# Kernel optimization log

Hardware: AMD Instinct MI355X
Metric: run time of the kernel (lower is better)

Reference implementation:

```python
import jax, jax.numpy as jnp
import numpy as np
import math

HEADS = 4
DIM_HEAD = 32
EPS = 1e-5

def _ln_channels(x):
    # LayerNorm over channel axis (axis=1) of NCHW, no affine (eps=1e-5)
    mu = jnp.mean(x, axis=1, keepdims=True)
    var = jnp.mean((x - mu) ** 2, axis=1, keepdims=True)
    return (x - mu) * jax.lax.rsqrt(var + EPS)

def setup_inputs() -> dict:
    key = jax.random.key(0)
    k1, k2, k3, k4 = jax.random.split(key, 4)
    dim, inner = 256, HEADS * DIM_HEAD
    x = jax.random.normal(k1, (16, dim, 64, 64), dtype=jnp.float32)
    Wqkv = jax.random.normal(k2, (3 * inner, dim), dtype=jnp.float32) * (1.0 / math.sqrt(dim))
    Wout = jax.random.normal(k3, (dim, inner), dtype=jnp.float32) * (1.0 / math.sqrt(inner))
    bout = jax.random.normal(k4, (dim,), dtype=jnp.float32) * 0.01
    return {"x": x, "Wqkv": Wqkv, "Wout": Wout, "bout": bout}

def reference(x, Wqkv, Wout, bout):
    B, C, H, W = x.shape
    N = H * W
    inner = HEADS * DIM_HEAD
    # pre-norm (channel-wise LayerNorm via permute in torch)
    normed = _ln_channels(x)
    # 1x1 conv to qkv: [B, 3*inner, H, W]
    qkv = jnp.einsum('oc,bchw->bohw', Wqkv, normed)
    q, k, v = jnp.split(qkv, 3, axis=1)
    # [B, inner, H, W] -> [B, heads, N, dim_head]
    def to_heads(t):
        return t.reshape(B, HEADS, DIM_HEAD, N).transpose(0, 1, 3, 2)
    q, k, v = to_heads(q), to_heads(k), to_heads(v)
    q = jax.nn.softmax(q, axis=-1)          # over dim_head
    k = jax.nn.softmax(k, axis=-2)          # over N
    q = q / math.sqrt(DIM_HEAD)
    v = v / N
    context = jnp.einsum('bhnd,bhne->bhde', k, v)   # [B,h,d,d]
    out = jnp.einsum('bhde,bhnd->bhne', context, q) # [B,h,N,d]
    out = out.transpose(0, 1, 3, 2).reshape(B, inner, H, W)
    out = jnp.einsum('oc,bchw->bohw', Wout, out) + bout[None, :, None, None]
    out = _ln_channels(out)                  # LinearAttention.out_norm
    return out + x                           # residual
```

## Files before the change

### kernel.cpp

```cpp
#include <hip/hip_runtime.h>
#include <hip/hip_bf16.h>
#include <math.h>

#define BATCH 16
#define CH 256
#define NPOS 4096
#define INNER 128
#define HEADS 4
#define DH 32

typedef __hip_bfloat16 bf16;
typedef short bf8v __attribute__((ext_vector_type(8)));
typedef float f32x4 __attribute__((ext_vector_type(4)));

__device__ __forceinline__ float b2f(bf16 v) { return __bfloat162float(v); }
__device__ __forceinline__ float us2f(unsigned short u) {
    unsigned w = ((unsigned)u) << 16; float f; __builtin_memcpy(&f, &w, 4); return f;
}
__device__ __forceinline__ unsigned short f2us(float f) {
    bf16 h = __float2bfloat16(f); unsigned short u; __builtin_memcpy(&u, &h, 2); return u;
}
__device__ __forceinline__ bf16 f2b(float v) { return __float2bfloat16(v); }

__global__ __launch_bounds__(256)
void prep_w_kernel(const float* __restrict__ Wqkv, bf16* __restrict__ wqb) {
    int idx = (blockIdx.x * 256 + threadIdx.x) * 4;
    float4 w = *(const float4*)&Wqkv[idx];
    ushort4 u;
    u.x = f2us(w.x); u.y = f2us(w.y); u.z = f2us(w.z); u.w = f2us(w.w);
    *(ushort4*)&wqb[idx] = u;
}

__global__ __launch_bounds__(256)
void fused_qkv_kernel(const float* __restrict__ x, const bf16* __restrict__ wqb,
                      bf16* __restrict__ p, bf16* __restrict__ kvt) {
    __shared__ bf16 A[64 * 264];
    __shared__ float stats[512];

    const int b = blockIdx.y, n0 = blockIdx.x * 64;
    const int tid = threadIdx.x;
    const int w = tid >> 6, lane = tid & 63;
    const int lrow = lane & 15, kq = lane >> 4;

    {
        const int n = tid & 63, cq = tid >> 6;
        const float* xp = x + ((size_t)b * CH + cq * 64) * NPOS + n0 + n;
        float s = 0.f, sq = 0.f;
        for (int i0 = 0; i0 < 64; i0 += 8) {
            bf8v bv;
            #pragma unroll
            for (int j = 0; j < 8; ++j) {
                float v = xp[(size_t)(i0 + j) * NPOS];
                s += v; sq += v * v;
                bv[j] = (short)f2us(v);
            }
            *(bf8v*)&A[n * 264 + cq * 64 + i0] = bv;
        }
        stats[tid * 2] = s; stats[tid * 2 + 1] = sq;
    }
    __syncthreads();
    if (tid < 64) {
        float s  = stats[tid * 2]     + stats[(tid + 64) * 2]
                 + stats[(tid + 128) * 2] + stats[(tid + 192) * 2];
        float sq = stats[tid * 2 + 1] + stats[(tid + 64) * 2 + 1]
                 + stats[(tid + 128) * 2 + 1] + stats[(tid + 192) * 2 + 1];
        float m = s * (1.f / 256.f);
        float var = sq * (1.f / 256.f) - m * m;
        stats[tid * 2] = m;
        stats[tid * 2 + 1] = rsqrtf(var + 1e-5f);
    }
    __syncthreads();
    {
        unsigned* A32 = (unsigned*)A;
        #pragma unroll 4
        for (int i = 0; i < 32; ++i) {
            int idx = i * 256 + tid;
            int c2 = idx & 127, n = idx >> 7;
            unsigned u = A32[n * 132 + c2];
            float m = stats[n * 2], rs = stats[n * 2 + 1];
            float v0 = (us2f((unsigned short)(u & 0xffffu)) - m) * rs;
            float v1 = (us2f((unsigned short)(u >> 16)) - m) * rs;
            A32[n * 132 + c2] = (unsigned)f2us(v0) | ((unsigned)f2us(v1) << 16);
        }
    }
    __syncthreads();

    for (int ph = 0; ph < 3; ++ph) {
        const int colbase = (ph == 2) ? 0 : (ph + 1) * 128;
        const bf16* wp = wqb + (size_t)(colbase + w * 32) * 256;
        f32x4 acc[4][2];
        #pragma unroll
        for (int i = 0; i < 4; ++i) {
            acc[i][0] = (f32x4){0.f, 0.f, 0.f, 0.f};
            acc[i][1] = (f32x4){0.f, 0.f, 0.f, 0.f};
        }

        #pragma unroll 2
        for (int k0 = 0; k0 < 256; k0 += 32) {
            bf8v af[4], bfr[2];
            #pragma unroll
            for (int t = 0; t < 4; ++t)
                af[t] = *(const bf8v*)&A[(t * 16 + lrow) * 264 + k0 + kq * 8];
            #pragma unroll
            for (int t = 0; t < 2; ++t)
                bfr[t] = *(const bf8v*)&wp[(size_t)(t * 16 + lrow) * 256 + k0 + kq * 8];
            #pragma unroll
            for (int mt = 0; mt < 4; ++mt)
                #pragma unroll
                for (int nt = 0; nt < 2; ++nt)
                    acc[mt][nt] = __builtin_amdgcn_mfma_f32_16x16x32_bf16(
                        af[mt], bfr[nt], acc[mt][nt], 0, 0, 0);
        }

        if (ph < 2) {
            #pragma unroll
            for (int mt = 0; mt < 4; ++mt)
                #pragma unroll
                for (int nt = 0; nt < 2; ++nt)
                    #pragma unroll
                    for (int r = 0; r < 4; ++r) {
                        int row = mt * 16 + kq * 4 + r;
                        int col = w * 32 + nt * 16 + lrow;
                        kvt[(size_t)(b * NPOS + n0 + row) * 256 + ph * 128 + col] =
                            f2b(acc[mt][nt][r]);
                    }
        } else {
            #pragma unroll
            for (int mt = 0; mt < 4; ++mt)
                #pragma unroll
                for (int r = 0; r < 4; ++r) {
                    float e0 = __expf(b2f(f2b(acc[mt][0][r])));
                    float e1 = __expf(b2f(f2b(acc[mt][1][r])));
                    float s = e0 + e1;
                    #pragma unroll
                    for (int m = 1; m <= 8; m <<= 1) s += __shfl_xor(s, m, 64);
                    float rd = 1.f / s;
                    int row = mt * 16 + kq * 4 + r;
                    bf16* pr_ = p + (size_t)(b * NPOS + n0 + row) * 128 + w * 32 + lrow;
                    pr_[0]  = f2b(e0 * rd);
                    pr_[16] = f2b(e1 * rd);
                }
        }
    }
}

__global__ __launch_bounds__(256)
void context_kernel(const bf16* __restrict__ kvt, float* __restrict__ ctxu,
                    float* __restrict__ separt) {
    __shared__ float ks[128][36];
    __shared__ float vs[128][36];
    __shared__ float red_se[4][32];
    int sp = blockIdx.x, h = blockIdx.y, b = blockIdx.z;
    int tid = threadIdx.x;
    int wave = tid >> 6, lane = tid & 63;
    int eg = lane & 7, dg = lane >> 3;
    int sd = tid & 31, sq = (tid >> 5) & 3;
    const int koff = h * DH, voff = 128 + h * DH;
    size_t rowbase = ((size_t)b * NPOS + sp * 1024) * 256;

    float acc[4][4] = {};
    float se_loc = 0.f;

    for (int nc = 0; nc < 1024; nc += 128) {
        for (int t = tid; t < 1024; t += 256) {
            int n = t >> 3, dq = t & 7;
            const bf16* row = kvt + rowbase + (size_t)(nc + n) * 256;
            ushort4 ku = *(const ushort4*)(row + koff + dq * 4);
            ushort4 vu = *(const ushort4*)(row + voff + dq * 4);
            f32x4 kf, vf;
            kf[0] = __expf(us2f(ku.x)); kf[1] = __expf(us2f(ku.y));
            kf[2] = __expf(us2f(ku.z)); kf[3] = __expf(us2f(ku.w));
            vf[0] = us2f(vu.x); vf[1] = us2f(vu.y); vf[2] = us2f(vu.z); vf[3] = us2f(vu.w);
            *(f32x4*)&ks[n][dq * 4] = kf;
            *(f32x4*)&vs[n][dq * 4] = vf;
        }
        __syncthreads();
        #pragma unroll 4
        for (int i = 0; i < 32; ++i) {
            int n = wave * 32 + i;
            f32x4 kv = *(const f32x4*)&ks[n][dg * 4];
            f32x4 vv = *(const f32x4*)&vs[n][eg * 4];
            #pragma unroll
            for (int j = 0; j < 4; ++j)
                #pragma unroll
                for (int i2 = 0; i2 < 4; ++i2)
                    acc[j][i2] += kv[j] * vv[i2];
        }
        if (tid < 128) {
            float s = 0.f;
            #pragma unroll 8
            for (int i = 0; i < 32; ++i) s += ks[sq * 32 + i][sd];
            se_loc += s;
        }
        __syncthreads();
    }

    if (tid < 128) red_se[sq][sd] = se_loc;
    float* red = &ks[0][0];
    #pragma unroll
    for (int j = 0; j < 4; ++j)
        #pragma unroll
        for (int i = 0; i < 4; ++i)
            red[(wave * 64 + lane) * 16 + j * 4 + i] = acc[j][i];
    __syncthreads();
    size_t bhsp = ((size_t)(b * HEADS + h) * 4 + sp);
    for (int idx = tid; idx < 1024; idx += 256) {
        int d = idx >> 5, e = idx & 31;
        int l = (d >> 2) * 8 + (e >> 2);
        int slot = (d & 3) * 4 + (e & 3);
        float s = 0.f;
        #pragma unroll
        for (int w = 0; w < 4; ++w) s += red[(w * 64 + l) * 16 + slot];
        ctxu[bhsp * 1024 + idx] = s;
    }
    if (tid < 32) {
        float s = red_se[0][tid] + red_se[1][tid] + red_se[2][tid] + red_se[3][tid];
        separt[bhsp * 32 + tid] = s;
    }
}

__global__ __launch_bounds__(256)
void wmod_kernel(const float* __restrict__ Wout, const float* __restrict__ ctxu,
                 const float* __restrict__ separt, bf16* __restrict__ wmod) {
    __shared__ float cs[4096];
    __shared__ float ses[128];
    int cg = blockIdx.x, b = blockIdx.y;
    int tid = threadIdx.x;
    for (int idx = tid; idx < 4096; idx += 256) {
        int hh = idx >> 10, rest = idx & 1023;
        float s = 0.f;
        #pragma unroll
        for (int sp = 0; sp < 4; ++sp)
            s += ctxu[(((size_t)(b * HEADS + hh) * 4) + sp) * 1024 + rest];
        cs[idx] = s;
    }
    if (tid < 128) {
        int hh = tid >> 5, d = tid & 31;
        float s = 0.f;
        #pragma unroll
        for (int sp = 0; sp < 4; ++sp)
            s += separt[(((size_t)(b * HEADS + hh) * 4) + sp) * 32 + d];
        ses[tid] = s;
    }
    __syncthreads();
    int c = cg * 32 + (tid & 31);
    int g = tid >> 5;
    int h = g >> 1, d0 = (g & 1) * 16;
    const float* wr = Wout + (size_t)c * INNER + h * DH;
    float w[32];
    #pragma unroll
    for (int i = 0; i < 8; ++i) {
        float4 t = *(const float4*)&wr[i * 4];
        w[i * 4] = t.x; w[i * 4 + 1] = t.y; w[i * 4 + 2] = t.z; w[i * 4 + 3] = t.w;
    }
    const float SCALE = 4.3158341e-05f;
    #pragma unroll
    for (int dd = 0; dd < 16; ++dd) {
        int d = d0 + dd;
        const float* cr = &cs[h * 1024 + d * 32];
        float s = 0.f;
        #pragma unroll
        for (int e4 = 0; e4 < 8; ++e4) {
            f32x4 t = *(const f32x4*)&cr[e4 * 4];
            s += w[e4 * 4] * t[0] + w[e4 * 4 + 1] * t[1]
               + w[e4 * 4 + 2] * t[2] + w[e4 * 4 + 3] * t[3];
        }
        float val = s * SCALE / ses[h * 32 + d];
        wmod[((size_t)b * CH + c) * INNER + h * DH + d] = f2b(val);
    }
}

__global__ __launch_bounds__(256)
void fused_out_kernel(const bf16* __restrict__ p, const bf16* __restrict__ wmod,
                      const float* __restrict__ bout, const float* __restrict__ x,
                      float* __restrict__ out) {
    __shared__ char lds[36864];
    bf16* Ap = (bf16*)lds;
    float* ct = (float*)lds;
    float* st = (float*)(lds + 33792);

    const int b = blockIdx.y, n0 = blockIdx.x * 64;
    const int tid = threadIdx.x;
    const int w = tid >> 6, lane = tid & 63;
    const int lrow = lane & 15, kq = lane >> 4;

    {
        const unsigned* pg32 = (const unsigned*)p;
        unsigned* A32 = (unsigned*)Ap;
        #pragma unroll 4
        for (int i = 0; i < 16; ++i) {
            int idx = i * 256 + tid;
            int c2 = idx & 63, n = idx >> 6;
            A32[n * 68 + c2] = pg32[(size_t)(b * NPOS + n0 + n) * 64 + c2];
        }
    }
    __syncthreads();

    f32x4 acc[4][4];
    #pragma unroll
    for (int i = 0; i < 4; ++i)
        #pragma unroll
        for (int j = 0; j < 4; ++j) acc[i][j] = (f32x4){0.f, 0.f, 0.f, 0.f};

    const bf16* wb = wmod + (size_t)b * CH * INNER + (size_t)(w * 64) * INNER;
    #pragma unroll 2
    for (int k0 = 0; k0 < 128; k0 += 32) {
        bf8v af[4], bfr[4];
        #pragma unroll
        for (int t = 0; t < 4; ++t)
            af[t] = *(const bf8v*)&Ap[(t * 16 + lrow) * 136 + k0 + kq * 8];
        #pragma unroll
        for (int t = 0; t < 4; ++t)
            bfr[t] = *(const bf8v*)&wb[(size_t)(t * 16 + lrow) * 128 + k0 + kq * 8];
        #pragma unroll
        for (int mt = 0; mt < 4; ++mt)
            #pragma unroll
            for (int nt = 0; nt < 4; ++nt)
                acc[mt][nt] = __builtin_amdgcn_mfma_f32_16x16x32_bf16(
                    af[mt], bfr[nt], acc[mt][nt], 0, 0, 0);
    }

    #pragma unroll
    for (int nt = 0; nt < 4; ++nt) {
        float bv = bout[w * 64 + nt * 16 + lrow];
        #pragma unroll
        for (int mt = 0; mt < 4; ++mt)
            #pragma unroll
            for (int r = 0; r < 4; ++r) acc[mt][nt][r] += bv;
    }

    #pragma unroll
    for (int mt = 0; mt < 4; ++mt)
        #pragma unroll
        for (int r = 0; r < 4; ++r) {
            float s = 0.f, sq = 0.f;
            #pragma unroll
            for (int nt = 0; nt < 4; ++nt) {
                float v = acc[mt][nt][r];
                s += v; sq += v * v;
            }
            #pragma unroll
            for (int m = 1; m <= 8; m <<= 1) {
                s += __shfl_xor(s, m, 64);
                sq += __shfl_xor(sq, m, 64);
            }
            if (lrow == 0) {
                int row = mt * 16 + kq * 4 + r;
                st[w * 128 + row * 2] = s;
                st[w * 128 + row * 2 + 1] = sq;
            }
        }
    __syncthreads();
    if (tid < 64) {
        float s  = st[tid * 2]     + st[128 + tid * 2]
                 + st[256 + tid * 2] + st[384 + tid * 2];
        float sq = st[tid * 2 + 1] + st[128 + tid * 2 + 1]
                 + st[256 + tid * 2 + 1] + st[384 + tid * 2 + 1];
        float m = s * (1.f / 256.f);
        float var = sq * (1.f / 256.f) - m * m;
        st[512 + tid * 2] = m;
        st[512 + tid * 2 + 1] = rsqrtf(var + 1e-5f);
    }
    __syncthreads();
    #pragma unroll
    for (int mt = 0; mt < 4; ++mt)
        #pragma unroll
        for (int r = 0; r < 4; ++r) {
            int row = mt * 16 + kq * 4 + r;
            float m = st[512 + row * 2], rs = st[512 + row * 2 + 1];
            #pragma unroll
            for (int nt = 0; nt < 4; ++nt)
                acc[mt][nt][r] = (acc[mt][nt][r] - m) * rs;
        }

    for (int pr = 0; pr < 2; ++pr) {
        __syncthreads();
        #pragma unroll
        for (int mi = 0; mi < 2; ++mi) {
            int mt = pr * 2 + mi;
            #pragma unroll
            for (int nt = 0; nt < 4; ++nt)
                #pragma unroll
                for (int r = 0; r < 4; ++r) {
                    int rl = mi * 16 + kq * 4 + r;
                    ct[(w * 64 + nt * 16 + lrow) * 33 + rl] = acc[mt][nt][r];
                }
        }
        __syncthreads();
        #pragma unroll 4
        for (int i = 0; i < 32; ++i) {
            int idx = i * 256 + tid;
            int n = idx & 31, c = idx >> 5;
            size_t gi = ((size_t)b * CH + c) * NPOS + n0 + pr * 32 + n;
            out[gi] = ct[c * 33 + n] + x[gi];
        }
    }
}

extern "C" void kernel_launch(void* const* d_in, const int* in_sizes, int n_in,
                              void* d_out, int out_size, void* d_ws, size_t ws_size,
                              hipStream_t stream) {
    const float* x    = (const float*)d_in[0];
    const float* Wqkv = (const float*)d_in[1];
    const float* Wout = (const float*)d_in[2];
    const float* bout = (const float*)d_in[3];
    float* out = (float*)d_out;

    char* ws = (char*)d_ws;
    bf16*  p      = (bf16*)ws;
    bf16*  kvt    = (bf16*)(ws + 16777216);
    float* ctxu   = (float*)(ws + 50331648);
    float* separt = (float*)(ws + 51380224);
    bf16*  wmod   = (bf16*)(ws + 51412992);
    bf16*  wqb    = (bf16*)(ws + 50331648);

    prep_w_kernel<<<dim3(96), 256, 0, stream>>>(Wqkv, wqb);
    fused_qkv_kernel<<<dim3(64, BATCH), 256, 0, stream>>>(x, wqb, p, kvt);
    context_kernel<<<dim3(4, HEADS, BATCH), 256, 0, stream>>>(kvt, ctxu, separt);
    wmod_kernel<<<dim3(8, BATCH), 256, 0, stream>>>(Wout, ctxu, separt, wmod);
    fused_out_kernel<<<dim3(64, BATCH), 256, 0, stream>>>(p, wmod, bout, x, out);
}
```

Before: 211.6 us.

## Fuse k/v context computation into QKV kernel via per-tile MFMA partials

```diff
diff --git a/kernel.cpp b/kernel.cpp
--- a/kernel.cpp
+++ b/kernel.cpp
@@ -33,41 +33,51 @@
 
 __global__ __launch_bounds__(256)
 void fused_qkv_kernel(const float* __restrict__ x, const bf16* __restrict__ wqb,
-                      bf16* __restrict__ p, bf16* __restrict__ kvt) {
-    __shared__ bf16 A[64 * 264];
-    __shared__ float stats[512];
-
-    const int b = blockIdx.y, n0 = blockIdx.x * 64;
+                      bf16* __restrict__ p, float* __restrict__ ctxp) {
+    __shared__ char smem[36864];
+    __shared__ float stats[640];
+
+    const int b = blockIdx.y, tile = blockIdx.x, n0 = tile * 64;
     const int tid = threadIdx.x;
     const int w = tid >> 6, lane = tid & 63;
     const int lrow = lane & 15, kq = lane >> 4;
+    bf16* A = (bf16*)smem;
 
     {
-        const int n = tid & 63, cq = tid >> 6;
-        const float* xp = x + ((size_t)b * CH + cq * 64) * NPOS + n0 + n;
-        float s = 0.f, sq = 0.f;
-        for (int i0 = 0; i0 < 64; i0 += 8) {
-            bf8v bv;
-            #pragma unroll
-            for (int j = 0; j < 8; ++j) {
-                float v = xp[(size_t)(i0 + j) * NPOS];
-                s += v; sq += v * v;
-                bv[j] = (short)f2us(v);
-            }
-            *(bf8v*)&A[n * 264 + cq * 64 + i0] = bv;
-        }
-        stats[tid * 2] = s; stats[tid * 2 + 1] = sq;
+        const int nq = tid & 15, cp = tid >> 4;
+        float s[4] = {0.f,0.f,0.f,0.f}, sq[4] = {0.f,0.f,0.f,0.f};
+        #pragma unroll
+        for (int i = 0; i < 8; ++i) {
+            int c0 = cp * 2 + 32 * i;
+            const float* xp = x + ((size_t)b * CH + c0) * NPOS + n0 + nq * 4;
+            float4 fa = *(const float4*)xp;
+            float4 fb = *(const float4*)(xp + NPOS);
+            #pragma unroll
+            for (int j = 0; j < 4; ++j) {
+                float va = (&fa.x)[j], vb = (&fb.x)[j];
+                s[j] += va + vb; sq[j] += va * va + vb * vb;
+                *(unsigned*)&A[(nq * 4 + j) * 264 + c0] =
+                    (unsigned)f2us(va) | ((unsigned)f2us(vb) << 16);
+            }
+        }
+        #pragma unroll
+        for (int j = 0; j < 4; ++j) {
+            s[j]  += __shfl_xor(s[j], 16, 64);  sq[j] += __shfl_xor(sq[j], 16, 64);
+            s[j]  += __shfl_xor(s[j], 32, 64);  sq[j] += __shfl_xor(sq[j], 32, 64);
+            if (lane < 16) {
+                stats[(nq * 4 + j) * 8 + w * 2]     = s[j];
+                stats[(nq * 4 + j) * 8 + w * 2 + 1] = sq[j];
+            }
+        }
     }
     __syncthreads();
     if (tid < 64) {
-        float s  = stats[tid * 2]     + stats[(tid + 64) * 2]
-                 + stats[(tid + 128) * 2] + stats[(tid + 192) * 2];
-        float sq = stats[tid * 2 + 1] + stats[(tid + 64) * 2 + 1]
-                 + stats[(tid + 128) * 2 + 1] + stats[(tid + 192) * 2 + 1];
+        float s  = stats[tid*8] + stats[tid*8+2] + stats[tid*8+4] + stats[tid*8+6];
+        float sq = stats[tid*8+1] + stats[tid*8+3] + stats[tid*8+5] + stats[tid*8+7];
         float m = s * (1.f / 256.f);
         float var = sq * (1.f / 256.f) - m * m;
-        stats[tid * 2] = m;
-        stats[tid * 2 + 1] = rsqrtf(var + 1e-5f);
+        stats[512 + tid * 2] = m;
+        stats[512 + tid * 2 + 1] = rsqrtf(var + 1e-5f);
     }
     __syncthreads();
     {
@@ -77,7 +87,7 @@
             int idx = i * 256 + tid;
             int c2 = idx & 127, n = idx >> 7;
             unsigned u = A32[n * 132 + c2];
-            float m = stats[n * 2], rs = stats[n * 2 + 1];
+            float m = stats[512 + n * 2], rs = stats[512 + n * 2 + 1];
             float v0 = (us2f((unsigned short)(u & 0xffffu)) - m) * rs;
             float v1 = (us2f((unsigned short)(u >> 16)) - m) * rs;
             A32[n * 132 + c2] = (unsigned)f2us(v0) | ((unsigned)f2us(v1) << 16);
@@ -85,16 +95,17 @@
     }
     __syncthreads();
 
+    ushort4 ekp[4][2];
+    float se0 = 0.f, se1 = 0.f;
+
     for (int ph = 0; ph < 3; ++ph) {
-        const int colbase = (ph == 2) ? 0 : (ph + 1) * 128;
-        const bf16* wp = wqb + (size_t)(colbase + w * 32) * 256;
+        const bf16* wp = wqb + (size_t)(ph * 128 + w * 32) * 256;
         f32x4 acc[4][2];
         #pragma unroll
         for (int i = 0; i < 4; ++i) {
-            acc[i][0] = (f32x4){0.f, 0.f, 0.f, 0.f};
-            acc[i][1] = (f32x4){0.f, 0.f, 0.f, 0.f};
-        }
-
+            acc[i][0] = (f32x4){0.f,0.f,0.f,0.f};
+            acc[i][1] = (f32x4){0.f,0.f,0.f,0.f};
+        }
         #pragma unroll 2
         for (int k0 = 0; k0 < 256; k0 += 32) {
             bf8v af[4], bfr[2];
@@ -112,19 +123,8 @@
                         af[mt], bfr[nt], acc[mt][nt], 0, 0, 0);
         }
 
-        if (ph < 2) {
-            #pragma unroll
-            for (int mt = 0; mt < 4; ++mt)
-                #pragma unroll
-                for (int nt = 0; nt < 2; ++nt)
-                    #pragma unroll
-                    for (int r = 0; r < 4; ++r) {
-                        int row = mt * 16 + kq * 4 + r;
-                        int col = w * 32 + nt * 16 + lrow;
-                        kvt[(size_t)(b * NPOS + n0 + row) * 256 + ph * 128 + col] =
-                            f2b(acc[mt][nt][r]);
-                    }
-        } else {
+        if (ph == 0) {
+            unsigned* pg32 = (unsigned*)p;
             #pragma unroll
             for (int mt = 0; mt < 4; ++mt)
                 #pragma unroll
@@ -132,90 +132,96 @@
                     float e0 = __expf(b2f(f2b(acc[mt][0][r])));
                     float e1 = __expf(b2f(f2b(acc[mt][1][r])));
                     float s = e0 + e1;
-                    #pragma unroll
-                    for (int m = 1; m <= 8; m <<= 1) s += __shfl_xor(s, m, 64);
+                    s += __shfl_xor(s, 1, 64);  s += __shfl_xor(s, 2, 64);
+                    s += __shfl_xor(s, 4, 64);  s += __shfl_xor(s, 8, 64);
                     float rd = 1.f / s;
                     int row = mt * 16 + kq * 4 + r;
-                    bf16* pr_ = p + (size_t)(b * NPOS + n0 + row) * 128 + w * 32 + lrow;
-                    pr_[0]  = f2b(e0 * rd);
-                    pr_[16] = f2b(e1 * rd);
+                    pg32[(size_t)(b * NPOS + n0 + row) * 64 + w * 16 + lrow] =
+                        (unsigned)f2us(e0 * rd) | ((unsigned)f2us(e1 * rd) << 16);
                 }
+        } else if (ph == 1) {
+            se0 = 0.f; se1 = 0.f;
+            #pragma unroll
+            for (int mt = 0; mt < 4; ++mt) {
+                ushort4 u0, u1;
+                unsigned short q_;
+                #pragma unroll
+                for (int r = 0; r < 4; ++r) {
+                    q_ = f2us(__expf(b2f(f2b(acc[mt][0][r]))));
+                    se0 += us2f(q_); (&u0.x)[r] = q_;
+                    q_ = f2us(__expf(b2f(f2b(acc[mt][1][r]))));
+                    se1 += us2f(q_); (&u1.x)[r] = q_;
+                }
+                ekp[mt][0] = u0; ekp[mt][1] = u1;
+            }
+            se0 += __shfl_xor(se0, 16, 64); se0 += __shfl_xor(se0, 32, 64);
+            se1 += __shfl_xor(se1, 16, 64); se1 += __shfl_xor(se1, 32, 64);
+        } else {
+            __syncthreads();
+            bf16* ekt = (bf16*)(smem + w * 9216);
+            bf16* vt  = (bf16*)(smem + w * 9216 + 4608);
+            #pragma unroll
+            for (int mt = 0; mt < 4; ++mt)
+                #pragma unroll
+                for (int nt = 0; nt < 2; ++nt) {
+                    ushort4 vv;
+                    vv.x = f2us(acc[mt][nt][0]); vv.y = f2us(acc[mt][nt][1]);
+                    vv.z = f2us(acc[mt][nt][2]); vv.w = f2us(acc[mt][nt][3]);
+                    int d = nt * 16 + lrow, n = mt * 16 + kq * 4;
+                    *(ushort4*)&vt[d * 72 + n]  = vv;
+                    *(ushort4*)&ekt[d * 72 + n] = ekp[mt][nt];
+                }
+            f32x4 cacc[2][2];
+            cacc[0][0] = (f32x4){0.f,0.f,0.f,0.f}; cacc[0][1] = cacc[0][0];
+            cacc[1][0] = cacc[0][0];               cacc[1][1] = cacc[0][0];
+            #pragma unroll
+            for (int ks = 0; ks < 2; ++ks) {
+                bf8v a2[2], bv2[2];
+                a2[0]  = *(const bf8v*)&ekt[lrow * 72 + ks * 32 + kq * 8];
+                a2[1]  = *(const bf8v*)&ekt[(16 + lrow) * 72 + ks * 32 + kq * 8];
+                bv2[0] = *(const bf8v*)&vt[lrow * 72 + ks * 32 + kq * 8];
+                bv2[1] = *(const bf8v*)&vt[(16 + lrow) * 72 + ks * 32 + kq * 8];
+                #pragma unroll
+                for (int mt2 = 0; mt2 < 2; ++mt2)
+                    #pragma unroll
+                    for (int nt2 = 0; nt2 < 2; ++nt2)
+                        cacc[mt2][nt2] = __builtin_amdgcn_mfma_f32_16x16x32_bf16(
+                            a2[mt2], bv2[nt2], cacc[mt2][nt2], 0, 0, 0);
+            }
+            float* pb = ctxp + ((size_t)(b * 64 + tile) * 4 + w) * 1056;
+            #pragma unroll
+            for (int mt2 = 0; mt2 < 2; ++mt2)
+                #pragma unroll
+                for (int nt2 = 0; nt2 < 2; ++nt2)
+                    #pragma unroll
+                    for (int r = 0; r < 4; ++r) {
+                        int d = mt2 * 16 + kq * 4 + r, e = nt2 * 16 + lrow;
+                        pb[d * 32 + e] = cacc[mt2][nt2][r];
+                    }
+            if (kq == 0) {
+                pb[1024 + lrow] = se0;
+                pb[1024 + 16 + lrow] = se1;
+            }
         }
     }
 }
 
 __global__ __launch_bounds__(256)
-void context_kernel(const bf16* __restrict__ kvt, float* __restrict__ ctxu,
-                    float* __restrict__ separt) {
-    __shared__ float ks[128][36];
-    __shared__ float vs[128][36];
-    __shared__ float red_se[4][32];
-    int sp = blockIdx.x, h = blockIdx.y, b = blockIdx.z;
+void reduce_ctx_kernel(const float* __restrict__ ctxp, float* __restrict__ ctxu,
+                       float* __restrict__ separt) {
+    int h = blockIdx.x, b = blockIdx.y;
     int tid = threadIdx.x;
-    int wave = tid >> 6, lane = tid & 63;
-    int eg = lane & 7, dg = lane >> 3;
-    int sd = tid & 31, sq = (tid >> 5) & 3;
-    const int koff = h * DH, voff = 128 + h * DH;
-    size_t rowbase = ((size_t)b * NPOS + sp * 1024) * 256;
-
-    float acc[4][4] = {};
-    float se_loc = 0.f;
-
-    for (int nc = 0; nc < 1024; nc += 128) {
-        for (int t = tid; t < 1024; t += 256) {
-            int n = t >> 3, dq = t & 7;
-            const bf16* row = kvt + rowbase + (size_t)(nc + n) * 256;
-            ushort4 ku = *(const ushort4*)(row + koff + dq * 4);
-            ushort4 vu = *(const ushort4*)(row + voff + dq * 4);
-            f32x4 kf, vf;
-            kf[0] = __expf(us2f(ku.x)); kf[1] = __expf(us2f(ku.y));
-            kf[2] = __expf(us2f(ku.z)); kf[3] = __expf(us2f(ku.w));
-            vf[0] = us2f(vu.x); vf[1] = us2f(vu.y); vf[2] = us2f(vu.z); vf[3] = us2f(vu.w);
-            *(f32x4*)&ks[n][dq * 4] = kf;
-            *(f32x4*)&vs[n][dq * 4] = vf;
-        }
-        __syncthreads();
-        #pragma unroll 4
-        for (int i = 0; i < 32; ++i) {
-            int n = wave * 32 + i;
-            f32x4 kv = *(const f32x4*)&ks[n][dg * 4];
-            f32x4 vv = *(const f32x4*)&vs[n][eg * 4];
-            #pragma unroll
-            for (int j = 0; j < 4; ++j)
-                #pragma unroll
-                for (int i2 = 0; i2 < 4; ++i2)
-                    acc[j][i2] += kv[j] * vv[i2];
-        }
-        if (tid < 128) {
-            float s = 0.f;
-            #pragma unroll 8
-            for (int i = 0; i < 32; ++i) s += ks[sq * 32 + i][sd];
-            se_loc += s;
-        }
-        __syncthreads();
-    }
-
-    if (tid < 128) red_se[sq][sd] = se_loc;
-    float* red = &ks[0][0];
-    #pragma unroll
-    for (int j = 0; j < 4; ++j)
-        #pragma unroll
-        for (int i = 0; i < 4; ++i)
-            red[(wave * 64 + lane) * 16 + j * 4 + i] = acc[j][i];
-    __syncthreads();
-    size_t bhsp = ((size_t)(b * HEADS + h) * 4 + sp);
-    for (int idx = tid; idx < 1024; idx += 256) {
-        int d = idx >> 5, e = idx & 31;
-        int l = (d >> 2) * 8 + (e >> 2);
-        int slot = (d & 3) * 4 + (e & 3);
-        float s = 0.f;
-        #pragma unroll
-        for (int w = 0; w < 4; ++w) s += red[(w * 64 + l) * 16 + slot];
-        ctxu[bhsp * 1024 + idx] = s;
-    }
-    if (tid < 32) {
-        float s = red_se[0][tid] + red_se[1][tid] + red_se[2][tid] + red_se[3][tid];
-        separt[bhsp * 32 + tid] = s;
+    for (int i = 0; i < 2; ++i) {
+        int idx = i * 256 + tid;
+        if (idx >= 264) break;
+        f32x4 s = (f32x4){0.f,0.f,0.f,0.f};
+        for (int t = 0; t < 64; ++t) {
+            const float* src = ctxp + ((size_t)(b * 64 + t) * 4 + h) * 1056 + idx * 4;
+            s += *(const f32x4*)src;
+        }
+        int j = idx * 4;
+        if (j < 1024) *(f32x4*)&ctxu[((size_t)(b * 4 + h)) * 1024 + j] = s;
+        else          *(f32x4*)&separt[((size_t)(b * 4 + h)) * 32 + (j - 1024)] = s;
     }
 }
 
@@ -228,19 +234,11 @@
     int tid = threadIdx.x;
     for (int idx = tid; idx < 4096; idx += 256) {
         int hh = idx >> 10, rest = idx & 1023;
-        float s = 0.f;
-        #pragma unroll
-        for (int sp = 0; sp < 4; ++sp)
-            s += ctxu[(((size_t)(b * HEADS + hh) * 4) + sp) * 1024 + rest];
-        cs[idx] = s;
+        cs[idx] = ctxu[((size_t)(b * 4 + hh)) * 1024 + rest];
     }
     if (tid < 128) {
         int hh = tid >> 5, d = tid & 31;
-        float s = 0.f;
-        #pragma unroll
-        for (int sp = 0; sp < 4; ++sp)
-            s += separt[(((size_t)(b * HEADS + hh) * 4) + sp) * 32 + d];
-        ses[tid] = s;
+        ses[tid] = separt[((size_t)(b * 4 + hh)) * 32 + d];
     }
     __syncthreads();
     int c = cg * 32 + (tid & 31);
@@ -266,7 +264,8 @@
                + w[e4 * 4 + 2] * t[2] + w[e4 * 4 + 3] * t[3];
         }
         float val = s * SCALE / ses[h * 32 + d];
-        wmod[((size_t)b * CH + c) * INNER + h * DH + d] = f2b(val);
+        wmod[((size_t)b * CH + c) * INNER + h * DH + ((d & 15) * 2 + (d >> 4))] =
+            f2b(val);
     }
 }
 
@@ -274,10 +273,10 @@
 void fused_out_kernel(const bf16* __restrict__ p, const bf16* __restrict__ wmod,
                       const float* __restrict__ bout, const float* __restrict__ x,
                       float* __restrict__ out) {
-    __shared__ char lds[36864];
+    __shared__ char lds[39424];
     bf16* Ap = (bf16*)lds;
     float* ct = (float*)lds;
-    float* st = (float*)(lds + 33792);
+    float* st = (float*)(lds + 36864);
 
     const int b = blockIdx.y, n0 = blockIdx.x * 64;
     const int tid = threadIdx.x;
@@ -285,13 +284,14 @@
     const int lrow = lane & 15, kq = lane >> 4;
 
     {
-        const unsigned* pg32 = (const unsigned*)p;
+        const uint4* pg = (const uint4*)p;
         unsigned* A32 = (unsigned*)Ap;
-        #pragma unroll 4
-        for (int i = 0; i < 16; ++i) {
+        #pragma unroll
+        for (int i = 0; i < 4; ++i) {
             int idx = i * 256 + tid;
-            int c2 = idx & 63, n = idx >> 6;
-            A32[n * 68 + c2] = pg32[(size_t)(b * NPOS + n0 + n) * 64 + c2];
+            int c4 = idx & 15, n = idx >> 4;
+            uint4 u = pg[(size_t)(b * NPOS + n0 + n) * 16 + c4];
+            *(uint4*)(A32 + n * 68 + c4 * 4) = u;
         }
     }
     __syncthreads();
@@ -352,9 +352,9 @@
         }
     __syncthreads();
     if (tid < 64) {
-        float s  = st[tid * 2]     + st[128 + tid * 2]
+        float s  = st[tid * 2]       + st[128 + tid * 2]
                  + st[256 + tid * 2] + st[384 + tid * 2];
-        float sq = st[tid * 2 + 1] + st[128 + tid * 2 + 1]
+        float sq = st[tid * 2 + 1]       + st[128 + tid * 2 + 1]
                  + st[256 + tid * 2 + 1] + st[384 + tid * 2 + 1];
         float m = s * (1.f / 256.f);
         float var = sq * (1.f / 256.f) - m * m;
@@ -383,16 +383,21 @@
                 #pragma unroll
                 for (int r = 0; r < 4; ++r) {
                     int rl = mi * 16 + kq * 4 + r;
-                    ct[(w * 64 + nt * 16 + lrow) * 33 + rl] = acc[mt][nt][r];
+                    ct[(w * 64 + nt * 16 + lrow) * 36 + rl] = acc[mt][nt][r];
                 }
         }
         __syncthreads();
-        #pragma unroll 4
-        for (int i = 0; i < 32; ++i) {
+        #pragma unroll
+        for (int i = 0; i < 8; ++i) {
             int idx = i * 256 + tid;
-            int n = idx & 31, c = idx >> 5;
-            size_t gi = ((size_t)b * CH + c) * NPOS + n0 + pr * 32 + n;
-            out[gi] = ct[c * 33 + n] + x[gi];
+            int n4 = (idx & 7) * 4, c = idx >> 3;
+            size_t gi = ((size_t)b * CH + c) * NPOS + n0 + pr * 32 + n4;
+            f32x4 cv = *(const f32x4*)&ct[c * 36 + n4];
+            float4 xv = *(const float4*)&x[gi];
+            float4 ov;
+            ov.x = cv[0] + xv.x; ov.y = cv[1] + xv.y;
+            ov.z = cv[2] + xv.z; ov.w = cv[3] + xv.w;
+            *(float4*)&out[gi] = ov;
         }
     }
 }
@@ -408,15 +413,15 @@
 
     char* ws = (char*)d_ws;
     bf16*  p      = (bf16*)ws;
-    bf16*  kvt    = (bf16*)(ws + 16777216);
-    float* ctxu   = (float*)(ws + 50331648);
-    float* separt = (float*)(ws + 51380224);
-    bf16*  wmod   = (bf16*)(ws + 51412992);
-    bf16*  wqb    = (bf16*)(ws + 50331648);
+    float* ctxp   = (float*)(ws + 16777216);
+    float* ctxu   = (float*)(ws + 34078720);
+    float* separt = (float*)(ws + 34340864);
+    bf16*  wmod   = (bf16*)(ws + 34349056);
+    bf16*  wqb    = (bf16*)(ws + 35397632);
 
     prep_w_kernel<<<dim3(96), 256, 0, stream>>>(Wqkv, wqb);
-    fused_qkv_kernel<<<dim3(64, BATCH), 256, 0, stream>>>(x, wqb, p, kvt);
-    context_kernel<<<dim3(4, HEADS, BATCH), 256, 0, stream>>>(kvt, ctxu, separt);
+    fused_qkv_kernel<<<dim3(64, BATCH), 256, 0, stream>>>(x, wqb, p, ctxp);
+    reduce_ctx_kernel<<<dim3(4, BATCH), 256, 0, stream>>>(ctxp, ctxu, separt);
     wmod_kernel<<<dim3(8, BATCH), 256, 0, stream>>>(Wout, ctxu, separt, wmod);
     fused_out_kernel<<<dim3(64, BATCH), 256, 0, stream>>>(p, wmod, bout, x, out);
 }
```

After: 194.0 us. 1.09x faster.
